# Kernel optimization log

Hardware: AMD Instinct MI355X
Metric: run time of the kernel (lower is better)

## Reference

```python
import jax, jax.numpy as jnp
import numpy as np

N_NODES = 8192
N_EDGES = 262144
D_FEAT = 512
NHID = 32
LATENT = 16


def setup_inputs() -> dict:
    key = jax.random.key(0)
    ks = jax.random.split(key, 12)
    inp = {
        "features": jax.random.normal(ks[0], (N_NODES, D_FEAT), dtype=jnp.float32),
        "edge_src": jax.random.randint(ks[1], (N_EDGES,), 0, N_NODES, dtype=jnp.int32),
        "edge_dst": jax.random.randint(ks[2], (N_EDGES,), 0, N_NODES, dtype=jnp.int32),
        "edge_weight": jax.random.uniform(ks[3], (N_EDGES,), dtype=jnp.float32),
        # GCEncoder params (GCNConv: out = A @ (x W) + b)
        "Wg1": jax.random.normal(ks[4], (D_FEAT, NHID), dtype=jnp.float32) / np.sqrt(D_FEAT),
        "bg1": jnp.zeros((NHID,), jnp.float32),
        "Wg2": jax.random.normal(ks[5], (NHID, LATENT), dtype=jnp.float32) / np.sqrt(NHID),
        "bg2": jnp.zeros((LATENT,), jnp.float32),
        # MLP encoder params
        "We1": jax.random.normal(ks[6], (D_FEAT, NHID), dtype=jnp.float32) / np.sqrt(D_FEAT),
        "be1": jnp.zeros((NHID,), jnp.float32),
        "We2": jax.random.normal(ks[7], (NHID, LATENT), dtype=jnp.float32) / np.sqrt(NHID),
        "be2": jnp.zeros((LATENT,), jnp.float32),
        # MLP decoder params (latent -> features)
        "Wd1": jax.random.normal(ks[8], (LATENT, NHID), dtype=jnp.float32) / np.sqrt(LATENT),
        "bd1": jnp.zeros((NHID,), jnp.float32),
        "Wd2": jax.random.normal(ks[9], (NHID, D_FEAT), dtype=jnp.float32) / np.sqrt(NHID),
        "bd2": jnp.zeros((D_FEAT,), jnp.float32),
    }
    return inp


def _gcn_conv(x, W, b, edge_src, edge_dst, edge_weight, n_nodes):
    # transform then sparse aggregate: A @ (x W) + b
    xw = x @ W                                   # [N, out]
    msg = xw[edge_src] * edge_weight[:, None]    # [E, out]
    agg = jax.ops.segment_sum(msg, edge_dst, num_segments=n_nodes)
    return agg + b


def reference(features, edge_src, edge_dst, edge_weight,
              Wg1, bg1, Wg2, bg2, We1, be1, We2, be2, Wd1, bd1, Wd2, bd2):
    n = features.shape[0]
    # GCEncoder (dropout p=0.0)
    h = jax.nn.relu(_gcn_conv(features, Wg1, bg1, edge_src, edge_dst, edge_weight, n))
    za = jax.nn.relu(_gcn_conv(h, Wg2, bg2, edge_src, edge_dst, edge_weight, n))
    # MLP encoder
    zx = jax.nn.relu(jax.nn.relu(features @ We1 + be1) @ We2 + be2)
    # concat latents
    z = jnp.concatenate([za, zx], axis=1)        # [N, 2*latent]
    # inner-product decoder: sigmoid(z z^T)  -> [N, N]
    adj_recon = jax.nn.sigmoid(z @ z.T)
    # feature decoder MLP
    feat_recon = jax.nn.relu(jax.nn.relu(zx @ Wd1 + bd1) @ Wd2 + bd2)
    return adj_recon, feat_recon, z
```

## Files before the change

kernel.cpp:

```cpp
#include <hip/hip_runtime.h>

typedef unsigned short ushort_t;
typedef __attribute__((ext_vector_type(8))) short short8;
typedef __attribute__((ext_vector_type(4))) float floatx4;
typedef __attribute__((ext_vector_type(2))) float floatx2;

#define N_NODES 8192
#define N_EDGES 262144
#define D_FEAT 512
#define NHID 32
#define LATENT 16

#define ADJ_OFF 0
#define FEAT_OFF (8192*8192)
#define Z_OFF (8192*8192 + 8192*512)

#define BCAP 128

static __device__ __forceinline__ ushort_t f2bf(float f) {
    unsigned int u = __float_as_uint(f);
    unsigned int r = u + 0x7fffu + ((u >> 16) & 1u);
    return (ushort_t)(r >> 16);
}

static __device__ __forceinline__ float fsig(float x) {
    float e = __builtin_amdgcn_exp2f(x * -1.44269504f);
    return __builtin_amdgcn_rcpf(1.f + e);
}

__global__ __launch_bounds__(256) void k_enc(const float* __restrict__ feat,
                                             const float* __restrict__ Wg1,
                                             const float* __restrict__ We1,
                                             const float* __restrict__ be1,
                                             const float* __restrict__ We2,
                                             const float* __restrict__ be2,
                                             float* __restrict__ xwg,
                                             float* __restrict__ zxf,
                                             int* __restrict__ cnt) {
    __shared__ float WL[32][64];
    __shared__ float FL[16][36];
    __shared__ float HE[16][33];
    int tid = threadIdx.x;
    int gid = blockIdx.x * 256 + tid;
    if (gid < N_NODES) cnt[gid] = 0;

    int n = tid >> 4;
    int cr = tid & 15;
    int m0 = blockIdx.x * 16;
    float acc[4] = {};

    for (int kt = 0; kt < 16; kt++) {
        __syncthreads();
        {
            int i = tid;
            #pragma unroll
            for (int j = 0; j < 8; j++, i += 256) {
                int k = i >> 6, c = i & 63;
                int kg = kt * 32 + k;
                WL[k][c] = (c < 32) ? Wg1[kg * 32 + c] : We1[kg * 32 + (c - 32)];
            }
        }
        if (tid < 128) {
            int nn = tid >> 3, q = tid & 7;
            float4 v = *(const float4*)(feat + (m0 + nn) * 512 + kt * 32 + q * 4);
            FL[nn][q * 4 + 0] = v.x; FL[nn][q * 4 + 1] = v.y;
            FL[nn][q * 4 + 2] = v.z; FL[nn][q * 4 + 3] = v.w;
        }
        __syncthreads();
        #pragma unroll 4
        for (int k = 0; k < 32; k++) {
            float4 w = *(const float4*)&WL[k][cr * 4];
            float f0 = FL[n][k];
            acc[0] += f0 * w.x; acc[1] += f0 * w.y;
            acc[2] += f0 * w.z; acc[3] += f0 * w.w;
        }
    }
    int cg = cr * 4;
    if (cg < 32) {
        float4 v = make_float4(acc[0], acc[1], acc[2], acc[3]);
        *(float4*)(xwg + (m0 + n) * 32 + cg) = v;
    } else {
        int hc = cg - 32;
        #pragma unroll
        for (int t = 0; t < 4; t++) {
            float v = acc[t] + be1[hc + t];
            HE[n][hc + t] = v > 0.f ? v : 0.f;
        }
    }
    __syncthreads();
    {
        int j = cr;
        float s = be2[j];
        #pragma unroll 8
        for (int cc = 0; cc < 32; cc++) s += HE[n][cc] * We2[cc * 16 + j];
        zxf[(m0 + n) * 16 + j] = s > 0.f ? s : 0.f;
    }
}

__global__ __launch_bounds__(256) void k_scatfeat(const int* __restrict__ esrc,
                                                  const int* __restrict__ edst,
                                                  const float* __restrict__ ew,
                                                  int* __restrict__ cnt,
                                                  int2* __restrict__ sedge,
                                                  const float* __restrict__ zxf,
                                                  const float* __restrict__ Wd1,
                                                  const float* __restrict__ bd1,
                                                  const float* __restrict__ Wd2,
                                                  const float* __restrict__ bd2,
                                                  float* __restrict__ outF) {
    __shared__ float ZL[16][17];
    __shared__ float HT[16][33];
    int tid = threadIdx.x;
    if (blockIdx.x < 1024) {
        int e = blockIdx.x * 256 + tid;
        int d = edst[e];
        int pos = atomicAdd(&cnt[d], 1);
        if (pos < BCAP)
            sedge[d * BCAP + pos] = make_int2(esrc[e], __float_as_int(ew[e]));
    } else {
        int m0 = (int)(blockIdx.x - 1024) * 16;
        {
            int n = tid >> 4, k = tid & 15;
            ZL[n][k] = zxf[(m0 + n) * 16 + k];
        }
        __syncthreads();
        {
            int o = tid * 2;
            int n = o >> 5, c = o & 31;
            float s0 = bd1[c], s1 = bd1[c + 1];
            #pragma unroll
            for (int k = 0; k < 16; k++) {
                float z = ZL[n][k];
                s0 += z * Wd1[k * 32 + c];
                s1 += z * Wd1[k * 32 + c + 1];
            }
            HT[n][c] = s0 > 0.f ? s0 : 0.f;
            HT[n][c + 1] = s1 > 0.f ? s1 : 0.f;
        }
        __syncthreads();
        int c2 = tid * 2;
        floatx2 acc[16];
        #pragma unroll
        for (int n = 0; n < 16; n++) acc[n] = (floatx2){0.f, 0.f};
        for (int k = 0; k < 32; k++) {
            float2 w = *(const float2*)(Wd2 + k * 512 + c2);
            #pragma unroll
            for (int n = 0; n < 16; n++) {
                float t = HT[n][k];
                acc[n].x += t * w.x;
                acc[n].y += t * w.y;
            }
        }
        float b0 = bd2[c2], b1 = bd2[c2 + 1];
        #pragma unroll
        for (int n = 0; n < 16; n++) {
            float s0 = acc[n].x + b0, s1 = acc[n].y + b1;
            s0 = s0 > 0.f ? s0 : 0.f;
            s1 = s1 > 0.f ? s1 : 0.f;
            floatx2 pk = {s0, s1};
            *(floatx2*)(outF + (size_t)(m0 + n) * 512 + c2) = pk;
        }
    }
}

__global__ __launch_bounds__(256) void k_agg1(const float* __restrict__ xwg,
                                              const int* __restrict__ cnt,
                                              const int2* __restrict__ sedge,
                                              const float* __restrict__ bg1,
                                              const float* __restrict__ Wg2,
                                              float* __restrict__ hw2) {
    __shared__ float hsh[8][33];
    int ln = threadIdx.x >> 5, c = threadIdx.x & 31;
    int n = blockIdx.x * 8 + ln;
    int st = n * BCAP, en = st + min(cnt[n], BCAP);
    float acc = 0.f;
    int i = st;
    for (; i + 4 <= en; i += 4) {
        int2 e0 = sedge[i], e1 = sedge[i + 1], e2 = sedge[i + 2], e3 = sedge[i + 3];
        float s0 = __int_as_float(e0.y) * xwg[e0.x * 32 + c];
        float s1 = __int_as_float(e1.y) * xwg[e1.x * 32 + c];
        float s2 = __int_as_float(e2.y) * xwg[e2.x * 32 + c];
        float s3 = __int_as_float(e3.y) * xwg[e3.x * 32 + c];
        acc += (s0 + s1) + (s2 + s3);
    }
    for (; i < en; i++) {
        int2 e = sedge[i];
        acc += __int_as_float(e.y) * xwg[e.x * 32 + c];
    }
    float h = acc + bg1[c];
    hsh[ln][c] = h > 0.f ? h : 0.f;
    __syncthreads();
    if (threadIdx.x < 128) {
        int l2 = threadIdx.x >> 4, j = threadIdx.x & 15;
        float s2 = 0.f;
        #pragma unroll 8
        for (int cc = 0; cc < 32; cc++) s2 += hsh[l2][cc] * Wg2[cc * 16 + j];
        hw2[(blockIdx.x * 8 + l2) * 16 + j] = s2;
    }
}

__global__ __launch_bounds__(256) void k_agg2(const float* __restrict__ hw2,
                                              const int* __restrict__ cnt,
                                              const int2* __restrict__ sedge,
                                              const float* __restrict__ bg2,
                                              const float* __restrict__ zxf,
                                              ushort_t* __restrict__ zbf,
                                              float* __restrict__ zout) {
    int ln = threadIdx.x >> 4, c = threadIdx.x & 15;
    int n = blockIdx.x * 16 + ln;
    int st = n * BCAP, en = st + min(cnt[n], BCAP);
    float acc = 0.f;
    int i = st;
    for (; i + 4 <= en; i += 4) {
        int2 e0 = sedge[i], e1 = sedge[i + 1], e2 = sedge[i + 2], e3 = sedge[i + 3];
        float s0 = __int_as_float(e0.y) * hw2[e0.x * 16 + c];
        float s1 = __int_as_float(e1.y) * hw2[e1.x * 16 + c];
        float s2 = __int_as_float(e2.y) * hw2[e2.x * 16 + c];
        float s3 = __int_as_float(e3.y) * hw2[e3.x * 16 + c];
        acc += (s0 + s1) + (s2 + s3);
    }
    for (; i < en; i++) {
        int2 e = sedge[i];
        acc += __int_as_float(e.y) * hw2[e.x * 16 + c];
    }
    float za = acc + bg2[c];
    za = za > 0.f ? za : 0.f;
    float zx = zxf[n * 16 + c];
    zout[n * 32 + c] = za;
    zout[n * 32 + 16 + c] = zx;
    zbf[n * 32 + c] = f2bf(za);
    zbf[n * 32 + 16 + c] = f2bf(zx);
}

__global__ __launch_bounds__(128) void k_adj(const ushort_t* __restrict__ zbf,
                                             float* __restrict__ adj) {
    __shared__ float TB[2][16][256];
    int tid = threadIdx.x;
    int l = tid & 63;
    int wv = tid >> 6;
    int strip = blockIdx.x & 15;
    int rt = (blockIdx.x >> 4) * 2 + wv;
    int q = l >> 4, cl = l & 15;
    int m0 = rt * 16, c0 = strip * 512;
    float (*T)[256] = TB[wv];

    short8 a = *(const short8*)(zbf + (m0 + cl) * 32 + q * 8);
    for (int half = 0; half < 2; half++) {
        int cb0 = c0 + half * 256;
        __syncthreads();
        #pragma unroll
        for (int g = 0; g < 4; g++) {
            int cb = cb0 + g * 64;
            short8 b0 = *(const short8*)(zbf + (cb + 4 * cl + 0) * 32 + q * 8);
            short8 b1 = *(const short8*)(zbf + (cb + 4 * cl + 1) * 32 + q * 8);
            short8 b2 = *(const short8*)(zbf + (cb + 4 * cl + 2) * 32 + q * 8);
            short8 b3 = *(const short8*)(zbf + (cb + 4 * cl + 3) * 32 + q * 8);
            floatx4 zv = {0, 0, 0, 0};
            floatx4 a0 = __builtin_amdgcn_mfma_f32_16x16x32_bf16(a, b0, zv, 0, 0, 0);
            floatx4 a1 = __builtin_amdgcn_mfma_f32_16x16x32_bf16(a, b1, zv, 0, 0, 0);
            floatx4 a2 = __builtin_amdgcn_mfma_f32_16x16x32_bf16(a, b2, zv, 0, 0, 0);
            floatx4 a3 = __builtin_amdgcn_mfma_f32_16x16x32_bf16(a, b3, zv, 0, 0, 0);
            #pragma unroll
            for (int r = 0; r < 4; r++) {
                floatx4 v;
                v.x = fsig(a0[r]);
                v.y = fsig(a1[r]);
                v.z = fsig(a2[r]);
                v.w = fsig(a3[r]);
                *(floatx4*)&T[q * 4 + r][g * 64 + 4 * cl] = v;
            }
        }
        __syncthreads();
        #pragma unroll 4
        for (int r = 0; r < 16; r++) {
            floatx4 v = *(const floatx4*)&T[r][4 * l];
            __builtin_nontemporal_store(v, (floatx4*)(adj + (size_t)(m0 + r) * 8192 + cb0 + 4 * l));
        }
    }
}

extern "C" void kernel_launch(void* const* d_in, const int* in_sizes, int n_in,
                              void* d_out, int out_size, void* d_ws, size_t ws_size,
                              hipStream_t stream) {
    const float* feat = (const float*)d_in[0];
    const int* esrc = (const int*)d_in[1];
    const int* edst = (const int*)d_in[2];
    const float* ew = (const float*)d_in[3];
    const float* Wg1 = (const float*)d_in[4];
    const float* bg1 = (const float*)d_in[5];
    const float* Wg2 = (const float*)d_in[6];
    const float* bg2 = (const float*)d_in[7];
    const float* We1 = (const float*)d_in[8];
    const float* be1 = (const float*)d_in[9];
    const float* We2 = (const float*)d_in[10];
    const float* be2 = (const float*)d_in[11];
    const float* Wd1 = (const float*)d_in[12];
    const float* bd1 = (const float*)d_in[13];
    const float* Wd2 = (const float*)d_in[14];
    const float* bd2 = (const float*)d_in[15];
    float* out = (float*)d_out;

    char* ws = (char*)d_ws;
    float* xwg      = (float*)(ws + 0);
    float* zxf      = (float*)(ws + 1048576);
    float* hw2      = (float*)(ws + 1572864);
    ushort_t* zbf   = (ushort_t*)(ws + 2097152);
    int* cnt        = (int*)(ws + 2621440);
    int2* sedge     = (int2*)(ws + 2654208);

    k_enc<<<N_NODES / 16, 256, 0, stream>>>(feat, Wg1, We1, be1, We2, be2,
                                            xwg, zxf, cnt);
    k_scatfeat<<<1024 + 512, 256, 0, stream>>>(esrc, edst, ew, cnt, sedge,
                                               zxf, Wd1, bd1, Wd2, bd2, out + FEAT_OFF);
    k_agg1<<<N_NODES / 8, 256, 0, stream>>>(xwg, cnt, sedge, bg1, Wg2, hw2);
    k_agg2<<<N_NODES / 16, 256, 0, stream>>>(hw2, cnt, sedge, bg2, zxf,
                                             zbf, out + Z_OFF);
    k_adj<<<(N_NODES / 16 / 2) * 16, 128, 0, stream>>>(zbf, out + ADJ_OFF);
}
```

Measured before the change: 428.5 us.

## Drop LDS staging in adjacency kernel and double rows per encoder block

The adjacency kernel no longer transposes its MFMA results through shared memory. Each lane now writes its sigmoid outputs straight to global memory in 256-byte row segments, using ordinary stores instead of nontemporal ones, with 4 waves per block. This removes the LDS round trip and barriers, at the cost of less coalesced, cache-allocating stores for the large N×N output. The encoder kernel now computes 32 nodes per block, two rows per thread, to reuse the weight tile loaded into shared memory and halve the block count.

```diff
diff --git a/kernel.cpp b/kernel.cpp
--- a/kernel.cpp
+++ b/kernel.cpp
@@ -38,16 +38,16 @@
                                              float* __restrict__ zxf,
                                              int* __restrict__ cnt) {
     __shared__ float WL[32][64];
-    __shared__ float FL[16][36];
-    __shared__ float HE[16][33];
+    __shared__ float FL[32][33];
+    __shared__ float HE[32][33];
     int tid = threadIdx.x;
     int gid = blockIdx.x * 256 + tid;
     if (gid < N_NODES) cnt[gid] = 0;
 
-    int n = tid >> 4;
     int cr = tid & 15;
-    int m0 = blockIdx.x * 16;
-    float acc[4] = {};
+    int nr = tid >> 4;
+    int m0 = blockIdx.x * 32;
+    float acc[2][4] = {};
 
     for (int kt = 0; kt < 16; kt++) {
         __syncthreads();
@@ -60,41 +60,54 @@
                 WL[k][c] = (c < 32) ? Wg1[kg * 32 + c] : We1[kg * 32 + (c - 32)];
             }
         }
-        if (tid < 128) {
-            int nn = tid >> 3, q = tid & 7;
-            float4 v = *(const float4*)(feat + (m0 + nn) * 512 + kt * 32 + q * 4);
-            FL[nn][q * 4 + 0] = v.x; FL[nn][q * 4 + 1] = v.y;
-            FL[nn][q * 4 + 2] = v.z; FL[nn][q * 4 + 3] = v.w;
+        {
+            int n = tid >> 3, q = tid & 7;
+            float4 v = *(const float4*)(feat + (m0 + n) * 512 + kt * 32 + q * 4);
+            FL[n][q * 4 + 0] = v.x; FL[n][q * 4 + 1] = v.y;
+            FL[n][q * 4 + 2] = v.z; FL[n][q * 4 + 3] = v.w;
         }
         __syncthreads();
         #pragma unroll 4
         for (int k = 0; k < 32; k++) {
             float4 w = *(const float4*)&WL[k][cr * 4];
-            float f0 = FL[n][k];
-            acc[0] += f0 * w.x; acc[1] += f0 * w.y;
-            acc[2] += f0 * w.z; acc[3] += f0 * w.w;
+            float f0 = FL[nr * 2 + 0][k];
+            float f1 = FL[nr * 2 + 1][k];
+            acc[0][0] += f0 * w.x; acc[0][1] += f0 * w.y;
+            acc[0][2] += f0 * w.z; acc[0][3] += f0 * w.w;
+            acc[1][0] += f1 * w.x; acc[1][1] += f1 * w.y;
+            acc[1][2] += f1 * w.z; acc[1][3] += f1 * w.w;
         }
     }
     int cg = cr * 4;
     if (cg < 32) {
-        float4 v = make_float4(acc[0], acc[1], acc[2], acc[3]);
-        *(float4*)(xwg + (m0 + n) * 32 + cg) = v;
+        #pragma unroll
+        for (int j = 0; j < 2; j++) {
+            float4 v = make_float4(acc[j][0], acc[j][1], acc[j][2], acc[j][3]);
+            *(float4*)(xwg + (m0 + nr * 2 + j) * 32 + cg) = v;
+        }
     } else {
         int hc = cg - 32;
         #pragma unroll
-        for (int t = 0; t < 4; t++) {
-            float v = acc[t] + be1[hc + t];
-            HE[n][hc + t] = v > 0.f ? v : 0.f;
+        for (int j = 0; j < 2; j++) {
+            #pragma unroll
+            for (int t = 0; t < 4; t++) {
+                float v = acc[j][t] + be1[hc + t];
+                HE[nr * 2 + j][hc + t] = v > 0.f ? v : 0.f;
+            }
         }
     }
     __syncthreads();
-    {
-        int j = cr;
-        float s = be2[j];
-        #pragma unroll 8
-        for (int cc = 0; cc < 32; cc++) s += HE[n][cc] * We2[cc * 16 + j];
-        zxf[(m0 + n) * 16 + j] = s > 0.f ? s : 0.f;
-    }
+    int n = tid >> 3, j0 = (tid & 7) * 2;
+    float s0 = be2[j0], s1 = be2[j0 + 1];
+    #pragma unroll 8
+    for (int cc = 0; cc < 32; cc++) {
+        float h = HE[n][cc];
+        s0 += h * We2[cc * 16 + j0];
+        s1 += h * We2[cc * 16 + j0 + 1];
+    }
+    s0 = s0 > 0.f ? s0 : 0.f;
+    s1 = s1 > 0.f ? s1 : 0.f;
+    *(float2*)(zxf + (m0 + n) * 16 + j0) = make_float2(s0, s1);
 }
 
 __global__ __launch_bounds__(256) void k_scatfeat(const int* __restrict__ esrc,
@@ -232,49 +245,36 @@
     zbf[n * 32 + 16 + c] = f2bf(zx);
 }
 
-__global__ __launch_bounds__(128) void k_adj(const ushort_t* __restrict__ zbf,
+__global__ __launch_bounds__(256) void k_adj(const ushort_t* __restrict__ zbf,
                                              float* __restrict__ adj) {
-    __shared__ float TB[2][16][256];
     int tid = threadIdx.x;
     int l = tid & 63;
     int wv = tid >> 6;
     int strip = blockIdx.x & 15;
-    int rt = (blockIdx.x >> 4) * 2 + wv;
+    int rt = (blockIdx.x >> 4) * 4 + wv;
     int q = l >> 4, cl = l & 15;
     int m0 = rt * 16, c0 = strip * 512;
-    float (*T)[256] = TB[wv];
-
     short8 a = *(const short8*)(zbf + (m0 + cl) * 32 + q * 8);
-    for (int half = 0; half < 2; half++) {
-        int cb0 = c0 + half * 256;
-        __syncthreads();
-        #pragma unroll
-        for (int g = 0; g < 4; g++) {
-            int cb = cb0 + g * 64;
-            short8 b0 = *(const short8*)(zbf + (cb + 4 * cl + 0) * 32 + q * 8);
-            short8 b1 = *(const short8*)(zbf + (cb + 4 * cl + 1) * 32 + q * 8);
-            short8 b2 = *(const short8*)(zbf + (cb + 4 * cl + 2) * 32 + q * 8);
-            short8 b3 = *(const short8*)(zbf + (cb + 4 * cl + 3) * 32 + q * 8);
-            floatx4 zv = {0, 0, 0, 0};
-            floatx4 a0 = __builtin_amdgcn_mfma_f32_16x16x32_bf16(a, b0, zv, 0, 0, 0);
-            floatx4 a1 = __builtin_amdgcn_mfma_f32_16x16x32_bf16(a, b1, zv, 0, 0, 0);
-            floatx4 a2 = __builtin_amdgcn_mfma_f32_16x16x32_bf16(a, b2, zv, 0, 0, 0);
-            floatx4 a3 = __builtin_amdgcn_mfma_f32_16x16x32_bf16(a, b3, zv, 0, 0, 0);
-            #pragma unroll
-            for (int r = 0; r < 4; r++) {
-                floatx4 v;
-                v.x = fsig(a0[r]);
-                v.y = fsig(a1[r]);
-                v.z = fsig(a2[r]);
-                v.w = fsig(a3[r]);
-                *(floatx4*)&T[q * 4 + r][g * 64 + 4 * cl] = v;
-            }
-        }
-        __syncthreads();
-        #pragma unroll 4
-        for (int r = 0; r < 16; r++) {
-            floatx4 v = *(const floatx4*)&T[r][4 * l];
-            __builtin_nontemporal_store(v, (floatx4*)(adj + (size_t)(m0 + r) * 8192 + cb0 + 4 * l));
+    for (int g = 0; g < 8; g++) {
+        int cb = c0 + g * 64;
+        short8 b0 = *(const short8*)(zbf + (cb + 4 * cl + 0) * 32 + q * 8);
+        short8 b1 = *(const short8*)(zbf + (cb + 4 * cl + 1) * 32 + q * 8);
+        short8 b2 = *(const short8*)(zbf + (cb + 4 * cl + 2) * 32 + q * 8);
+        short8 b3 = *(const short8*)(zbf + (cb + 4 * cl + 3) * 32 + q * 8);
+        floatx4 zv = {0, 0, 0, 0};
+        floatx4 a0 = __builtin_amdgcn_mfma_f32_16x16x32_bf16(a, b0, zv, 0, 0, 0);
+        floatx4 a1 = __builtin_amdgcn_mfma_f32_16x16x32_bf16(a, b1, zv, 0, 0, 0);
+        floatx4 a2 = __builtin_amdgcn_mfma_f32_16x16x32_bf16(a, b2, zv, 0, 0, 0);
+        floatx4 a3 = __builtin_amdgcn_mfma_f32_16x16x32_bf16(a, b3, zv, 0, 0, 0);
+        #pragma unroll
+        for (int r = 0; r < 4; r++) {
+            floatx4 v;
+            v.x = fsig(a0[r]);
+            v.y = fsig(a1[r]);
+            v.z = fsig(a2[r]);
+            v.w = fsig(a3[r]);
+            int row = m0 + q * 4 + r;
+            *(floatx4*)(adj + (size_t)row * 8192 + cb + 4 * cl) = v;
         }
     }
 }
@@ -308,12 +308,12 @@
     int* cnt        = (int*)(ws + 2621440);
     int2* sedge     = (int2*)(ws + 2654208);
 
-    k_enc<<<N_NODES / 16, 256, 0, stream>>>(feat, Wg1, We1, be1, We2, be2,
+    k_enc<<<N_NODES / 32, 256, 0, stream>>>(feat, Wg1, We1, be1, We2, be2,
                                             xwg, zxf, cnt);
     k_scatfeat<<<1024 + 512, 256, 0, stream>>>(esrc, edst, ew, cnt, sedge,
                                                zxf, Wd1, bd1, Wd2, bd2, out + FEAT_OFF);
     k_agg1<<<N_NODES / 8, 256, 0, stream>>>(xwg, cnt, sedge, bg1, Wg2, hw2);
     k_agg2<<<N_NODES / 16, 256, 0, stream>>>(hw2, cnt, sedge, bg2, zxf,
                                              zbf, out + Z_OFF);
-    k_adj<<<(N_NODES / 16 / 2) * 16, 128, 0, stream>>>(zbf, out + ADJ_OFF);
-}
+    k_adj<<<(N_NODES / 16 / 4) * 16, 256, 0, stream>>>(zbf, out + ADJ_OFF);
+}
```

After: 433.7 us. About the same (+1.2%).
